# Kernel optimization log

Measured on AMD Instinct MI355X. Metric: run time of the kernel, lower is better.

Reference implementation:

```python
import jax, jax.numpy as jnp
import numpy as np
from jax import lax

BN_EPS = 1e-5

def _dw_conv_bn(img, w, g, b, mu, var):
    # img: [B,C,H,W], w: [C,1,3,3] depthwise (feature_group_count=C), stride 1, pad 1
    C = img.shape[1]
    y = lax.conv_general_dilated(img, w, (1, 1), 'SAME',
                                 dimension_numbers=('NCHW', 'OIHW', 'NCHW'),
                                 feature_group_count=C)
    scale = (g / jnp.sqrt(var + BN_EPS))[None, :, None, None]
    return y * scale + (b - mu * g / jnp.sqrt(var + BN_EPS))[None, :, None, None]


def setup_inputs() -> dict:
    key = jax.random.key(0)
    B, H, W, C, Co = 32, 28, 28, 192, 192
    T = 1 + H * W
    ks = jax.random.split(key, 8)
    x = jax.random.normal(ks[0], (B, T, C), dtype=jnp.float32)
    conv_w = jax.random.normal(ks[1], (3, C, 1, 3, 3), dtype=jnp.float32) * 0.1
    bn_scale = 1.0 + 0.1 * jax.random.normal(ks[2], (3, C), dtype=jnp.float32)
    bn_bias = 0.1 * jax.random.normal(ks[3], (3, C), dtype=jnp.float32)
    bn_mean = 0.1 * jax.random.normal(ks[4], (3, C), dtype=jnp.float32)
    bn_var = jax.random.uniform(ks[5], (3, C), dtype=jnp.float32, minval=0.5, maxval=1.5)
    w_qkv = jax.random.normal(ks[6], (3, Co, C), dtype=jnp.float32) / np.sqrt(C)
    kp, kb = jax.random.split(ks[7])
    w_proj = jax.random.normal(kp, (Co, Co), dtype=jnp.float32) / np.sqrt(Co)
    b_proj = 0.01 * jax.random.normal(kb, (Co,), dtype=jnp.float32)
    return {"x": x, "conv_w": conv_w, "bn_scale": bn_scale, "bn_bias": bn_bias,
            "bn_mean": bn_mean, "bn_var": bn_var, "w_qkv": w_qkv,
            "w_proj": w_proj, "b_proj": b_proj, "h": H, "w": W, "num_heads": 3}


def reference(x, conv_w, bn_scale, bn_bias, bn_mean, bn_var, w_qkv, w_proj, b_proj, h, w, num_heads):
    B, T, C = x.shape
    Co = w_proj.shape[0]
    scale = Co ** (-0.5)  # NOTE: module scales by dim_out^-0.5, not per-head
    cls_tok, tok = x[:, :1], x[:, 1:]
    img = tok.reshape(B, h, w, C).transpose(0, 3, 1, 2)  # b (h w) c -> b c h w
    qkv = []
    for i in range(3):  # q, k, v conv projections (depthwise conv + BN inference)
        y = _dw_conv_bn(img, conv_w[i], bn_scale[i], bn_bias[i], bn_mean[i], bn_var[i])
        y = y.reshape(B, C, h * w).transpose(0, 2, 1)  # b c h w -> b (h w) c
        y = jnp.concatenate([cls_tok, y], axis=1)      # prepend cls token
        qkv.append(jnp.einsum('btc,oc->bto', y, w_qkv[i]))
    d = Co // num_heads
    q, k, v = (t.reshape(B, T, num_heads, d).transpose(0, 2, 1, 3) for t in qkv)
    attn = jnp.einsum('bhld,bhtd->bhlt', q, k) * scale
    attn = jax.nn.softmax(attn, axis=-1)
    out = jnp.einsum('bhlt,bhtd->bhld', attn, v)
    out = out.transpose(0, 2, 1, 3).reshape(B, T, Co)
    return out @ w_proj.T + b_proj
```

## Files before the change

kernel.cpp:

```cpp
#include <hip/hip_runtime.h>

#define B_   32
#define Hh   28
#define Ww   28
#define Cc   192
#define T_   785
#define BT_  (B_ * T_)
#define BTC_ ((size_t)BT_ * Cc)
#define SCALE2 0.10412163388f

typedef __attribute__((ext_vector_type(8))) __bf16 bf16x8;
typedef __attribute__((ext_vector_type(4))) __bf16 bf16x4;
typedef __attribute__((ext_vector_type(4))) float  f32x4;

__global__ __launch_bounds__(192) void conv3_bn_k(
    const float* __restrict__ x, const float* __restrict__ cw,
    const float* __restrict__ g, const float* __restrict__ bb,
    const float* __restrict__ mu, const float* __restrict__ var,
    __bf16* __restrict__ y,
    const float* __restrict__ wqkv, const float* __restrict__ wproj,
    __bf16* __restrict__ wdst)
{
  const int c = threadIdx.x;
  const int bx = blockIdx.x;
  const int b = blockIdx.y;
  if (bx == 7) {
    int t = b * 192 + c;
    int base = t * 24;
    const float* src = (base < 3 * Cc * Cc) ? (wqkv + base)
                                            : (wproj + (base - 3 * Cc * Cc));
#pragma unroll
    for (int e = 0; e < 24; e += 4) {
      float4 v = *(const float4*)(src + e);
      wdst[base + e + 0] = (__bf16)v.x;
      wdst[base + e + 1] = (__bf16)v.y;
      wdst[base + e + 2] = (__bf16)v.z;
      wdst[base + e + 3] = (__bf16)v.w;
    }
    return;
  }
  const int h0 = bx * 4;
  float w9[3][9], sc[3], sh[3];
#pragma unroll
  for (int br = 0; br < 3; ++br) {
    sc[br] = g[br * Cc + c] * rsqrtf(var[br * Cc + c] + 1e-5f);
    sh[br] = bb[br * Cc + c] - mu[br * Cc + c] * sc[br];
#pragma unroll
    for (int k = 0; k < 9; ++k) w9[br][k] = cw[(br * Cc + c) * 9 + k];
  }
  const float* xb = x + (size_t)b * T_ * Cc;
  if (bx == 0) {
#pragma unroll
    for (int br = 0; br < 3; ++br)
      y[br * BTC_ + (size_t)b * T_ * Cc + c] = (__bf16)xb[c];
  }
  float c0[6], c1[6], c2[6];
#pragma unroll
  for (int r = 0; r < 6; ++r) {
    int rr = h0 - 1 + r;
    c0[r] = 0.f;
    c1[r] = (rr >= 0 && rr < Hh) ? xb[(size_t)(1 + rr * Ww) * Cc + c] : 0.f;
  }
  for (int col = 0; col < Ww; ++col) {
#pragma unroll
    for (int r = 0; r < 6; ++r) {
      int rr = h0 - 1 + r, ci = col + 1;
      c2[r] = (rr >= 0 && rr < Hh && ci < Ww)
                ? xb[(size_t)(1 + rr * Ww + ci) * Cc + c] : 0.f;
    }
#pragma unroll
    for (int ro = 0; ro < 4; ++ro) {
      size_t orow = (size_t)(b * T_ + 1 + (h0 + ro) * Ww + col) * Cc + c;
#pragma unroll
      for (int br = 0; br < 3; ++br) {
        float acc = c0[ro+0]*w9[br][0] + c1[ro+0]*w9[br][1] + c2[ro+0]*w9[br][2]
                  + c0[ro+1]*w9[br][3] + c1[ro+1]*w9[br][4] + c2[ro+1]*w9[br][5]
                  + c0[ro+2]*w9[br][6] + c1[ro+2]*w9[br][7] + c2[ro+2]*w9[br][8];
        y[br * BTC_ + orow] = (__bf16)(acc * sc[br] + sh[br]);
      }
    }
#pragma unroll
    for (int r = 0; r < 6; ++r) { c0[r] = c1[r]; c1[r] = c2[r]; }
  }
}

template <int MODE>
__global__ __launch_bounds__(512) void gemm_bf16(
    const __bf16* __restrict__ A0, const __bf16* __restrict__ W0,
    const float* __restrict__ bias, void* __restrict__ outp)
{
  __shared__ __bf16 As[128][72];
  __shared__ __bf16 Bs[192][72];
  const int z = blockIdx.z;
  const __bf16* A  = A0 + (MODE == 0 ? (size_t)z * BTC_ : 0);
  const __bf16* Bw = W0 + (MODE == 0 ? (size_t)z * Cc * Cc : 0);
  const float osc = (MODE == 0 && z == 0) ? SCALE2 : 1.0f;
  const int tid = threadIdx.x;
  const int wid = tid >> 6, l = tid & 63, c = l & 15, g = l >> 4;
  const int wm = wid >> 2, wn = wid & 3;
  const int m0 = blockIdx.x * 128;
  const int ar = tid >> 2, aq = tid & 3;
  const int brow = tid >> 3, bv = tid & 7;

  f32x4 acc[4][3];
#pragma unroll
  for (int i = 0; i < 4; ++i)
#pragma unroll
    for (int j = 0; j < 3; ++j) acc[i][j] = (f32x4)(0.f);

  const __bf16* ap = A + (size_t)(m0 + ar) * Cc + aq * 16;
  const __bf16* bp0 = Bw + (size_t)brow * Cc + bv * 8;
  uint4 a0 = *(const uint4*)(ap + 0);
  uint4 a1 = *(const uint4*)(ap + 8);
  uint4 b0 = *(const uint4*)(bp0);
  uint4 b1 = *(const uint4*)(bp0 + (size_t)64 * Cc);
  uint4 b2 = *(const uint4*)(bp0 + (size_t)128 * Cc);

  for (int kc = 0; kc < 3; ++kc) {
    __syncthreads();
    *(uint4*)&As[ar][aq * 16 + 0] = a0;
    *(uint4*)&As[ar][aq * 16 + 8] = a1;
    *(uint4*)&Bs[brow +   0][bv * 8] = b0;
    *(uint4*)&Bs[brow +  64][bv * 8] = b1;
    *(uint4*)&Bs[brow + 128][bv * 8] = b2;
    if (kc < 2) {
      ap += 64; bp0 += 64;
      a0 = *(const uint4*)(ap + 0);
      a1 = *(const uint4*)(ap + 8);
      b0 = *(const uint4*)(bp0);
      b1 = *(const uint4*)(bp0 + (size_t)64 * Cc);
      b2 = *(const uint4*)(bp0 + (size_t)128 * Cc);
    }
    __syncthreads();
#pragma unroll
    for (int ksl = 0; ksl < 2; ++ksl) {
      bf16x8 af[4], bfr[3];
#pragma unroll
      for (int mf = 0; mf < 4; ++mf)
        af[mf] = *(const bf16x8*)&As[wm * 64 + mf * 16 + c][ksl * 32 + g * 8];
#pragma unroll
      for (int nf = 0; nf < 3; ++nf)
        bfr[nf] = *(const bf16x8*)&Bs[wn * 48 + nf * 16 + c][ksl * 32 + g * 8];
      __builtin_amdgcn_s_setprio(1);
#pragma unroll
      for (int mf = 0; mf < 4; ++mf)
#pragma unroll
        for (int nf = 0; nf < 3; ++nf)
          acc[mf][nf] = __builtin_amdgcn_mfma_f32_16x16x32_bf16(
              af[mf], bfr[nf], acc[mf][nf], 0, 0, 0);
      __builtin_amdgcn_s_setprio(0);
    }
  }
  float bias_c[3] = {0.f, 0.f, 0.f};
  if (MODE == 1) {
#pragma unroll
    for (int nf = 0; nf < 3; ++nf) bias_c[nf] = bias[wn * 48 + nf * 16 + c];
  }
#pragma unroll
  for (int mf = 0; mf < 4; ++mf) {
#pragma unroll
    for (int i = 0; i < 4; ++i) {
      int m = m0 + wm * 64 + mf * 16 + g * 4 + i;
      if (m < BT_) {
#pragma unroll
        for (int nf = 0; nf < 3; ++nf) {
          int n = wn * 48 + nf * 16 + c;
          if (MODE == 1)
            ((float*)outp)[(size_t)m * Cc + n] = acc[mf][nf][i] + bias_c[nf];
          else
            ((__bf16*)outp)[z * BTC_ + (size_t)m * Cc + n] =
                (__bf16)(acc[mf][nf][i] * osc);
        }
      }
    }
  }
}

__global__ __launch_bounds__(256) void attn_mfma(
    const __bf16* __restrict__ qkv, __bf16* __restrict__ aout)
{
  __shared__ __bf16 Ks[2][64][72];
  __shared__ __bf16 Vt[2][64][72];
  __shared__ __bf16 Ps[4][16][72];
  const int bid = blockIdx.x;
  const int swz = (bid & 7) * 156 + (bid >> 3);
  const int qt = swz % 13;
  const int g2 = swz / 13;
  const int hh = g2 % 3;
  const int b  = g2 / 3;
  const int tid = threadIdx.x;
  const int wid = tid >> 6, l = tid & 63, c = l & 15, g = l >> 4;
  const __bf16* Q = qkv + ((size_t)(0 * B_ + b) * T_) * Cc + hh * 64;
  const __bf16* K = qkv + ((size_t)(1 * B_ + b) * T_) * Cc + hh * 64;
  const __bf16* V = qkv + ((size_t)(2 * B_ + b) * T_) * Cc + hh * 64;

  const int qrow = qt * 64 + wid * 16 + c;
  const __bf16* qp = Q + (size_t)qrow * Cc + g * 8;
  bf16x8 qf0 = *(const bf16x8*)(qp);
  bf16x8 qf1 = *(const bf16x8*)(qp + 32);

  const int skey = tid >> 2, sdq = tid & 3;
  const int vkp = tid & 31, vd0 = (tid >> 5) * 8;
  const __bf16* kp  = K + (size_t)skey * Cc + sdq * 16;
  const __bf16* vp0 = V + (size_t)(2 * vkp + 0) * Cc + vd0;
  const __bf16* vp1 = V + (size_t)(2 * vkp + 1) * Cc + vd0;

  uint4 kr0, kr1, va, vb;
  auto loadKV = [&]() {
    kr0 = *(const uint4*)(kp + 0);
    kr1 = *(const uint4*)(kp + 8);
    va  = *(const uint4*)vp0;
    vb  = *(const uint4*)vp1;
    kp += 64 * Cc; vp0 += 64 * Cc; vp1 += 64 * Cc;
  };
  auto writeLDS = [&](int buf) {
    *(uint4*)&Ks[buf][skey][sdq * 16 + 0] = kr0;
    *(uint4*)&Ks[buf][skey][sdq * 16 + 8] = kr1;
    const ushort* pa = (const ushort*)&va;
    const ushort* pb = (const ushort*)&vb;
#pragma unroll
    for (int e = 0; e < 8; ++e) {
      unsigned pk2 = (unsigned)pa[e] | ((unsigned)pb[e] << 16);
      *(unsigned*)&Vt[buf][vd0 + e][2 * vkp] = pk2;
    }
  };

  loadKV();
  writeLDS(0);
  loadKV();
  __syncthreads();

  f32x4 ot[4];
#pragma unroll
  for (int f = 0; f < 4; ++f) ot[f] = (f32x4)(0.f);
  float m_run = -1e30f, l_run = 0.f;

  for (int kt = 0; kt < 13; ++kt) {
    const int cur = kt & 1;
    if (kt < 12) {
      writeLDS(cur ^ 1);
      if (kt < 11) loadKV();
    }

    f32x4 st[4];
#pragma unroll
    for (int f = 0; f < 4; ++f) st[f] = (f32x4)(0.f);
    __builtin_amdgcn_s_setprio(1);
#pragma unroll
    for (int f = 0; f < 4; ++f) {
      bf16x8 ka = *(const bf16x8*)&Ks[cur][f * 16 + c][g * 8];
      st[f] = __builtin_amdgcn_mfma_f32_16x16x32_bf16(ka, qf0, st[f], 0, 0, 0);
    }
#pragma unroll
    for (int f = 0; f < 4; ++f) {
      bf16x8 ka = *(const bf16x8*)&Ks[cur][f * 16 + c][32 + g * 8];
      st[f] = __builtin_amdgcn_mfma_f32_16x16x32_bf16(ka, qf1, st[f], 0, 0, 0);
    }
    __builtin_amdgcn_s_setprio(0);

    if (kt == 12) {
#pragma unroll
      for (int f = 0; f < 4; ++f)
#pragma unroll
        for (int i = 0; i < 4; ++i)
          if (f * 16 + g * 4 + i >= 17) st[f][i] = -1e30f;
    }
    float pmax = -1e30f;
#pragma unroll
    for (int f = 0; f < 4; ++f)
#pragma unroll
      for (int i = 0; i < 4; ++i) pmax = fmaxf(pmax, st[f][i]);
    pmax = fmaxf(pmax, __shfl_xor(pmax, 16));
    pmax = fmaxf(pmax, __shfl_xor(pmax, 32));
    if (!__all(pmax <= m_run + 8.f)) {
      float mnew = fmaxf(m_run, pmax);
      float corr = exp2f(m_run - mnew);
      m_run = mnew;
      l_run *= corr;
#pragma unroll
      for (int f = 0; f < 4; ++f)
#pragma unroll
        for (int i = 0; i < 4; ++i) ot[f][i] *= corr;
    }
    float rs = 0.f;
#pragma unroll
    for (int f = 0; f < 4; ++f) {
      bf16x4 pk;
#pragma unroll
      for (int i = 0; i < 4; ++i) {
        float p = exp2f(st[f][i] - m_run);
        rs += p;
        pk[i] = (__bf16)p;
      }
      *(bf16x4*)&Ps[wid][c][f * 16 + g * 4] = pk;
    }
    rs += __shfl_xor(rs, 16);
    rs += __shfl_xor(rs, 32);
    l_run += rs;

    __builtin_amdgcn_s_setprio(1);
#pragma unroll
    for (int s2 = 0; s2 < 2; ++s2) {
      bf16x8 pb2 = *(const bf16x8*)&Ps[wid][c][s2 * 32 + g * 8];
#pragma unroll
      for (int f = 0; f < 4; ++f) {
        bf16x8 va2 = *(const bf16x8*)&Vt[cur][f * 16 + c][s2 * 32 + g * 8];
        ot[f] = __builtin_amdgcn_mfma_f32_16x16x32_bf16(va2, pb2, ot[f], 0, 0, 0);
      }
    }
    __builtin_amdgcn_s_setprio(0);
    __syncthreads();
  }

  const int t = qt * 64 + wid * 16 + c;
  if (t < T_) {
    float inv = 1.f / l_run;
    __bf16* op = aout + ((size_t)(b * T_ + t)) * Cc + hh * 64;
#pragma unroll
    for (int f = 0; f < 4; ++f) {
      bf16x4 ov;
#pragma unroll
      for (int i = 0; i < 4; ++i) ov[i] = (__bf16)(ot[f][i] * inv);
      *(bf16x4*)(op + f * 16 + g * 4) = ov;
    }
  }
}

extern "C" void kernel_launch(void* const* d_in, const int* in_sizes, int n_in,
                              void* d_out, int out_size, void* d_ws, size_t ws_size,
                              hipStream_t stream) {
  (void)in_sizes; (void)n_in; (void)out_size; (void)ws_size;
  const float* x        = (const float*)d_in[0];
  const float* conv_w   = (const float*)d_in[1];
  const float* bn_scale = (const float*)d_in[2];
  const float* bn_bias  = (const float*)d_in[3];
  const float* bn_mean  = (const float*)d_in[4];
  const float* bn_var   = (const float*)d_in[5];
  const float* w_qkv    = (const float*)d_in[6];
  const float* w_proj   = (const float*)d_in[7];
  const float* b_proj   = (const float*)d_in[8];

  __bf16* ybf  = (__bf16*)d_ws;
  __bf16* qkvb = ybf + 3 * BTC_;
  __bf16* aobf = qkvb + 3 * BTC_;
  __bf16* wq   = aobf + BTC_;
  __bf16* wp   = wq + 3 * Cc * Cc;

  conv3_bn_k<<<dim3(8, B_), 192, 0, stream>>>(
      x, conv_w, bn_scale, bn_bias, bn_mean, bn_var, ybf, w_qkv, w_proj, wq);

  const int mblocks = (BT_ + 127) / 128;
  gemm_bf16<0><<<dim3(mblocks, 1, 3), 512, 0, stream>>>(ybf, wq, nullptr, qkvb);
  attn_mfma<<<1248, 256, 0, stream>>>(qkvb, aobf);
  gemm_bf16<1><<<dim3(mblocks, 1, 1), 512, 0, stream>>>(aobf, wp, b_proj, d_out);
}
```

Baseline: 177.0 us.

## Single-buffer attention K/V tiles and drop register prefetch pipeline

The attention kernel swaps the double-buffered K/V LDS tiles with register prefetch for a single buffer. Each iteration now loads, writes and syncs before computing. This halves K/V shared memory and frees prefetch registers, which may raise occupancy, but global-load latency is no longer hidden behind compute. It also packs the V transpose with byte-permute instructions, uses a tree max reduction, and removes the s_setprio hints in the GEMM kernel.

```diff
diff --git a/kernel.cpp b/kernel.cpp
--- a/kernel.cpp
+++ b/kernel.cpp
@@ -141,14 +141,12 @@
 #pragma unroll
       for (int nf = 0; nf < 3; ++nf)
         bfr[nf] = *(const bf16x8*)&Bs[wn * 48 + nf * 16 + c][ksl * 32 + g * 8];
-      __builtin_amdgcn_s_setprio(1);
 #pragma unroll
       for (int mf = 0; mf < 4; ++mf)
 #pragma unroll
         for (int nf = 0; nf < 3; ++nf)
           acc[mf][nf] = __builtin_amdgcn_mfma_f32_16x16x32_bf16(
               af[mf], bfr[nf], acc[mf][nf], 0, 0, 0);
-      __builtin_amdgcn_s_setprio(0);
     }
   }
   float bias_c[3] = {0.f, 0.f, 0.f};
@@ -179,8 +177,8 @@
 __global__ __launch_bounds__(256) void attn_mfma(
     const __bf16* __restrict__ qkv, __bf16* __restrict__ aout)
 {
-  __shared__ __bf16 Ks[2][64][72];
-  __shared__ __bf16 Vt[2][64][72];
+  __shared__ __bf16 Ks[64][72];
+  __shared__ __bf16 Vt[64][72];
   __shared__ __bf16 Ps[4][16][72];
   const int bid = blockIdx.x;
   const int swz = (bid & 7) * 156 + (bid >> 3);
@@ -205,42 +203,32 @@
   const __bf16* vp0 = V + (size_t)(2 * vkp + 0) * Cc + vd0;
   const __bf16* vp1 = V + (size_t)(2 * vkp + 1) * Cc + vd0;
 
-  uint4 kr0, kr1, va, vb;
-  auto loadKV = [&]() {
-    kr0 = *(const uint4*)(kp + 0);
-    kr1 = *(const uint4*)(kp + 8);
-    va  = *(const uint4*)vp0;
-    vb  = *(const uint4*)vp1;
-    kp += 64 * Cc; vp0 += 64 * Cc; vp1 += 64 * Cc;
-  };
-  auto writeLDS = [&](int buf) {
-    *(uint4*)&Ks[buf][skey][sdq * 16 + 0] = kr0;
-    *(uint4*)&Ks[buf][skey][sdq * 16 + 8] = kr1;
-    const ushort* pa = (const ushort*)&va;
-    const ushort* pb = (const ushort*)&vb;
-#pragma unroll
-    for (int e = 0; e < 8; ++e) {
-      unsigned pk2 = (unsigned)pa[e] | ((unsigned)pb[e] << 16);
-      *(unsigned*)&Vt[buf][vd0 + e][2 * vkp] = pk2;
-    }
-  };
-
-  loadKV();
-  writeLDS(0);
-  loadKV();
-  __syncthreads();
-
   f32x4 ot[4];
 #pragma unroll
   for (int f = 0; f < 4; ++f) ot[f] = (f32x4)(0.f);
   float m_run = -1e30f, l_run = 0.f;
 
   for (int kt = 0; kt < 13; ++kt) {
-    const int cur = kt & 1;
-    if (kt < 12) {
-      writeLDS(cur ^ 1);
-      if (kt < 11) loadKV();
-    }
+    __syncthreads();
+    {
+      uint4 kr0 = *(const uint4*)(kp + 0);
+      uint4 kr1 = *(const uint4*)(kp + 8);
+      uint4 va  = *(const uint4*)vp0;
+      uint4 vb  = *(const uint4*)vp1;
+      kp += 64 * Cc; vp0 += 64 * Cc; vp1 += 64 * Cc;
+      *(uint4*)&Ks[skey][sdq * 16 + 0] = kr0;
+      *(uint4*)&Ks[skey][sdq * 16 + 8] = kr1;
+      const unsigned* aw = (const unsigned*)&va;
+      const unsigned* bw = (const unsigned*)&vb;
+#pragma unroll
+      for (int w = 0; w < 4; ++w) {
+        unsigned lo = __builtin_amdgcn_perm(bw[w], aw[w], 0x05040100u);
+        unsigned hi = __builtin_amdgcn_perm(bw[w], aw[w], 0x07060302u);
+        *(unsigned*)&Vt[vd0 + 2 * w + 0][2 * vkp] = lo;
+        *(unsigned*)&Vt[vd0 + 2 * w + 1][2 * vkp] = hi;
+      }
+    }
+    __syncthreads();
 
     f32x4 st[4];
 #pragma unroll
@@ -248,12 +236,12 @@
     __builtin_amdgcn_s_setprio(1);
 #pragma unroll
     for (int f = 0; f < 4; ++f) {
-      bf16x8 ka = *(const bf16x8*)&Ks[cur][f * 16 + c][g * 8];
+      bf16x8 ka = *(const bf16x8*)&Ks[f * 16 + c][g * 8];
       st[f] = __builtin_amdgcn_mfma_f32_16x16x32_bf16(ka, qf0, st[f], 0, 0, 0);
     }
 #pragma unroll
     for (int f = 0; f < 4; ++f) {
-      bf16x8 ka = *(const bf16x8*)&Ks[cur][f * 16 + c][32 + g * 8];
+      bf16x8 ka = *(const bf16x8*)&Ks[f * 16 + c][32 + g * 8];
       st[f] = __builtin_amdgcn_mfma_f32_16x16x32_bf16(ka, qf1, st[f], 0, 0, 0);
     }
     __builtin_amdgcn_s_setprio(0);
@@ -265,11 +253,11 @@
         for (int i = 0; i < 4; ++i)
           if (f * 16 + g * 4 + i >= 17) st[f][i] = -1e30f;
     }
-    float pmax = -1e30f;
-#pragma unroll
-    for (int f = 0; f < 4; ++f)
-#pragma unroll
-      for (int i = 0; i < 4; ++i) pmax = fmaxf(pmax, st[f][i]);
+    float m01 = fmaxf(fmaxf(st[0][0], st[0][1]), fmaxf(st[0][2], st[0][3]));
+    float m11 = fmaxf(fmaxf(st[1][0], st[1][1]), fmaxf(st[1][2], st[1][3]));
+    float m21 = fmaxf(fmaxf(st[2][0], st[2][1]), fmaxf(st[2][2], st[2][3]));
+    float m31 = fmaxf(fmaxf(st[3][0], st[3][1]), fmaxf(st[3][2], st[3][3]));
+    float pmax = fmaxf(fmaxf(m01, m11), fmaxf(m21, m31));
     pmax = fmaxf(pmax, __shfl_xor(pmax, 16));
     pmax = fmaxf(pmax, __shfl_xor(pmax, 32));
     if (!__all(pmax <= m_run + 8.f)) {
@@ -304,12 +292,11 @@
       bf16x8 pb2 = *(const bf16x8*)&Ps[wid][c][s2 * 32 + g * 8];
 #pragma unroll
       for (int f = 0; f < 4; ++f) {
-        bf16x8 va2 = *(const bf16x8*)&Vt[cur][f * 16 + c][s2 * 32 + g * 8];
+        bf16x8 va2 = *(const bf16x8*)&Vt[f * 16 + c][s2 * 32 + g * 8];
         ot[f] = __builtin_amdgcn_mfma_f32_16x16x32_bf16(va2, pb2, ot[f], 0, 0, 0);
       }
     }
     __builtin_amdgcn_s_setprio(0);
-    __syncthreads();
   }
 
   const int t = qt * 64 + wid * 16 + c;
```

Measured after the change: 176.7 us. No clear change (-0.2%).
